# Optimization experiments

Hardware: AMD Instinct MI355X
Metric: run time of the kernel (lower is better)

## Reference

```python
import jax, jax.numpy as jnp
import numpy as np

EMB = 256
HEADS = 8
D_HEAD = EMB // HEADS


def apply_rope(x):
    # x: [B, H, T, D] (interleaved-pair RoPE, matching the torch source)
    T, D = x.shape[-2], x.shape[-1]
    freqs = 10000.0 ** (-jnp.arange(0, D, 2, dtype=jnp.float32) / D)  # [D/2]
    angles = jnp.arange(T, dtype=jnp.float32)[:, None] * freqs[None, :]  # [T, D/2]
    sin = jnp.repeat(jnp.sin(angles), 2, axis=1)  # [T, D]
    cos = jnp.repeat(jnp.cos(angles), 2, axis=1)  # [T, D]
    x1 = x[..., 0::2]
    x2 = x[..., 1::2]
    rotated = jnp.stack((-x2, x1), axis=-1).reshape(x.shape)  # interleave (-x2, x1)
    return x * cos + rotated * sin


def setup_inputs() -> dict:
    key = jax.random.key(0)
    k1, k2, k3, k4, k5 = jax.random.split(key, 5)
    B, T = 8, 2048
    x = jax.random.normal(k1, (B, T, EMB), dtype=jnp.float32)
    s = 1.0 / np.sqrt(EMB)
    # Linear weights stored as [in, out] (torch weight.T), y = x @ W + b
    Wqkv = jax.random.uniform(k2, (EMB, 3 * EMB), minval=-s, maxval=s, dtype=jnp.float32)
    bqkv = jax.random.uniform(k3, (3 * EMB,), minval=-s, maxval=s, dtype=jnp.float32)
    Wout = jax.random.uniform(k4, (EMB, EMB), minval=-s, maxval=s, dtype=jnp.float32)
    bout = jax.random.uniform(k5, (EMB,), minval=-s, maxval=s, dtype=jnp.float32)
    return {"x": x, "Wqkv": Wqkv, "bqkv": bqkv, "Wout": Wout, "bout": bout}


def reference(x, Wqkv, bqkv, Wout, bout):
    B, T, E = x.shape
    H, Dh = HEADS, D_HEAD
    qkv = x @ Wqkv + bqkv  # [B, T, 3E]
    qkv = qkv.reshape(B, T, 3, H, Dh).transpose(2, 0, 3, 1, 4)  # [3, B, H, T, Dh]
    q, k, v = qkv[0], qkv[1], qkv[2]
    q = apply_rope(q)
    k = apply_rope(k)
    scores = jnp.einsum('bhtd,bhsd->bhts', q, k) / np.sqrt(Dh)  # [B, H, T, T]
    causal = jnp.triu(jnp.ones((T, T), dtype=bool), k=1)
    scores = jnp.where(causal, -jnp.inf, scores)
    attn = jax.nn.softmax(scores, axis=-1)
    out = jnp.einsum('bhts,bhsd->bthd', attn, v).reshape(B, T, E)
    return out @ Wout + bout
```

## Files before the change

kernel.cpp:

```cpp
#include <hip/hip_runtime.h>
#include <hip/hip_bf16.h>
#include <math.h>

typedef __hip_bfloat16 bf16;
using s8v = __attribute__((ext_vector_type(8))) short;
using f4v = __attribute__((ext_vector_type(4))) float;
using u32x2 = __attribute__((ext_vector_type(2))) unsigned int;

#if __has_builtin(__builtin_amdgcn_exp2f)
#define EXP2(x) __builtin_amdgcn_exp2f(x)
#else
#define EXP2(x) exp2f(x)
#endif

__device__ __forceinline__ float bfb2f(unsigned short u) {
    return __uint_as_float(((unsigned int)u) << 16);
}
__device__ __forceinline__ unsigned short f2bfb(float f) {
    unsigned int u = __float_as_uint(f);
    unsigned int r = (u + 0x7fffu + ((u >> 16) & 1u)) >> 16;
    return (unsigned short)r;
}
__device__ __forceinline__ unsigned int packbf2_rne(float a, float b) {
    return (unsigned int)f2bfb(a) | ((unsigned int)f2bfb(b) << 16);
}
__device__ __forceinline__ unsigned int packbf2(float a, float b) {
    return __builtin_amdgcn_perm(__float_as_uint(b) + 0x8000u,
                                 __float_as_uint(a) + 0x8000u,
                                 0x07060302u);
}
__device__ __forceinline__ s8v mk8(unsigned int a, unsigned int b,
                                   unsigned int c, unsigned int d) {
    union { unsigned int u[4]; s8v v; } x;
    x.u[0] = a; x.u[1] = b; x.u[2] = c; x.u[3] = d;
    return x.v;
}
__device__ __forceinline__ void plswap(unsigned int& a, unsigned int& b) {
    u32x2 t = __builtin_amdgcn_permlane32_swap(a, b, false, false);
    u32x2 u = __builtin_amdgcn_permlane16_swap(t.x, t.y, false, false);
    a = u.x;
    b = u.y;
}

__device__ __forceinline__ void gload_lds16(const void* g, void* l) {
    __builtin_amdgcn_global_load_lds(
        (const __attribute__((address_space(1))) unsigned int*)g,
        (__attribute__((address_space(3))) unsigned int*)l, 16, 0, 0);
}

__device__ __forceinline__ int sniff_fp32(const void* p, int tid, int* s_flag)
{
    if (tid == 0) *s_flag = 0;
    __syncthreads();
    const uint4* u = (const uint4*)p;
    int local = 0;
    #pragma unroll
    for (int i = 0; i < 4; i++) {
        const uint4 v = u[i * 256 + tid];
        if ((v.x & 0x7F80u) == 0x7F80u) local = 1;
        if ((v.y & 0x7F80u) == 0x7F80u) local = 1;
        if ((v.z & 0x7F80u) == 0x7F80u) local = 1;
        if ((v.w & 0x7F80u) == 0x7F80u) local = 1;
    }
    if (local) atomicOr(s_flag, 1);
    __syncthreads();
    return *s_flag;
}

__global__ __launch_bounds__(256)
void k_prep(const void* __restrict__ x, const void* __restrict__ Wqkv,
            const void* __restrict__ bqkv, const void* __restrict__ Wout,
            const void* __restrict__ bout,
            bf16* __restrict__ wqkvT, bf16* __restrict__ woutT,
            float* __restrict__ bq_f, float* __restrict__ bo_f,
            bf16* __restrict__ xb)
{
    __shared__ int sf;
    const int bid = blockIdx.x;
    const int tid = threadIdx.x;
    if (bid < 768) {
        const int f = sniff_fp32(Wqkv, tid, &sf);
        unsigned short v = f ? f2bfb(((const float*)Wqkv)[(size_t)tid * 768 + bid])
                             : ((const unsigned short*)Wqkv)[(size_t)tid * 768 + bid];
        ((unsigned short*)wqkvT)[(size_t)bid * 256 + tid] = v;
        if (bid < 12) {
            const int i = bid * 256 + tid;
            bq_f[i] = f ? ((const float*)bqkv)[i]
                        : bfb2f(((const unsigned short*)bqkv)[i]);
        }
    } else if (bid < 1024) {
        const int n = bid - 768;
        const int f = sniff_fp32(Wout, tid, &sf);
        unsigned short v = f ? f2bfb(((const float*)Wout)[(size_t)tid * 256 + n])
                             : ((const unsigned short*)Wout)[(size_t)tid * 256 + n];
        ((unsigned short*)woutT)[(size_t)n * 256 + tid] = v;
        if (n == 0)
            bo_f[tid] = f ? ((const float*)bout)[tid]
                          : bfb2f(((const unsigned short*)bout)[tid]);
    } else {
        const int f = sniff_fp32(x, tid, &sf);
        if (f) {
            const size_t cb = (size_t)(bid - 1024) * 4096;
            #pragma unroll
            for (int i = 0; i < 4; i++) {
                const size_t e = cb + (size_t)i * 1024 + tid * 4;
                const float4 v = *(const float4*)((const float*)x + e);
                ushort4 o4;
                o4.x = f2bfb(v.x);
                o4.y = f2bfb(v.y);
                o4.z = f2bfb(v.z);
                o4.w = f2bfb(v.w);
                *(ushort4*)((unsigned short*)xb + e) = o4;
            }
        } else {
            const size_t base = (size_t)(bid - 1024) * 4096 + (size_t)tid * 16;
            const uint4* xu = (const uint4*)((const unsigned short*)x + base);
            uint4* dp = (uint4*)((unsigned short*)xb + base);
            dp[0] = xu[0];
            dp[1] = xu[1];
        }
    }
}

__global__ __launch_bounds__(256)
void k_qkv_rope(const bf16* __restrict__ xb, const bf16* __restrict__ wqkvT,
                const float* __restrict__ bq_f,
                bf16* __restrict__ q_ws, bf16* __restrict__ k_ws,
                bf16* __restrict__ vT_ws)
{
    __shared__ __align__(16) unsigned short Bls[4][8][512];
    __shared__ __align__(16) unsigned short Tls[4][1536];

    const int tid = threadIdx.x;
    const int bx = blockIdx.x;
    const int by = blockIdx.y;
    const int n0 = bx * 64;

    const int w    = tid >> 6;
    const int lane = tid & 63;
    const int col  = lane & 15;
    const int quad = lane >> 4;
    const int which = n0 >> 8;
    const int b     = (by * 128) >> 11;
    unsigned short* Tw = Tls[w];

    #pragma unroll
    for (int kk = 0; kk < 8; kk++)
        gload_lds16((const unsigned short*)wqkvT +
                        (size_t)(n0 + w * 16 + col) * 256 + kk * 32 + quad * 8,
                    &Bls[w][kk][0]);
    __syncthreads();

    const int T0 = by * 128 + w * 32;

    f4v acc[2][4] = {{{0.f,0.f,0.f,0.f}, {0.f,0.f,0.f,0.f},
                      {0.f,0.f,0.f,0.f}, {0.f,0.f,0.f,0.f}},
                     {{0.f,0.f,0.f,0.f}, {0.f,0.f,0.f,0.f},
                      {0.f,0.f,0.f,0.f}, {0.f,0.f,0.f,0.f}}};

    #pragma unroll
    for (int kk = 0; kk < 8; kk++) {
        const s8v av0 = *(const s8v*)((const unsigned short*)xb +
                        (size_t)(T0 + col) * 256 + kk * 32 + quad * 8);
        const s8v av1 = *(const s8v*)((const unsigned short*)xb +
                        (size_t)(T0 + 16 + col) * 256 + kk * 32 + quad * 8);
        #pragma unroll
        for (int c = 0; c < 4; c++) {
            const s8v bv = *(const s8v*)&Bls[c][kk][lane * 8];
            acc[0][c] = __builtin_amdgcn_mfma_f32_16x16x32_bf16(av0, bv, acc[0][c], 0, 0, 0);
            acc[1][c] = __builtin_amdgcn_mfma_f32_16x16x32_bf16(av1, bv, acc[1][c], 0, 0, 0);
        }
    }

    #pragma unroll
    for (int g = 0; g < 2; g++) {
        const int t_base = ((by * 128) & 2047) + w * 32 + g * 16;

        if (which == 2) {
            #pragma unroll
            for (int c = 0; c < 4; c++) {
                const int nl = c * 16 + col;
                const float bias = bq_f[n0 + nl];
                uint2 ww;
                ww.x = packbf2_rne(acc[g][c][0] + bias, acc[g][c][1] + bias);
                ww.y = packbf2_rne(acc[g][c][2] + bias, acc[g][c][3] + bias);
                *(uint2*)(Tw + nl * 24 + quad * 4) = ww;
            }
            const int ng = n0 + lane;
            const int h = (ng & 255) >> 5;
            const int d = ng & 31;
            const s8v t0 = *(const s8v*)&Tw[lane * 24];
            const s8v t1 = *(const s8v*)&Tw[lane * 24 + 8];
            unsigned short* dp = (unsigned short*)vT_ws +
                ((size_t)(b * 8 + h) * 32 + d) * 2048 + t_base;
            *(s8v*)dp = t0;
            *(s8v*)(dp + 8) = t1;
        } else {
            #pragma unroll
            for (int c = 0; c < 4; c++) {
                const int nl = c * 16 + col;
                const int d = (n0 + nl) & 31;
                const float bias = bq_f[n0 + nl];
                const float frev = __expf(-0.28782314f * (float)(d & ~1))
                                 * 0.15915494309189535f;
                #pragma unroll
                for (int r = 0; r < 4; r++) {
                    const float v = acc[g][c][r] + bias;
                    const float vp = __shfl_xor(v, 1);
                    const int t = t_base + quad * 4 + r;
                    float rev = (float)t * frev;
                    rev -= floorf(rev);
                    const float ang = rev * 6.283185307179586f;
                    const float sn = __sinf(ang);
                    const float cs = __cosf(ang);
                    float o = (d & 1) ? (v * cs + vp * sn)
                                      : (v * cs - vp * sn);
                    if (which == 0) o *= 0.25503487021228657f;
                    Tw[(quad * 4 + r) * 80 + nl] = f2bfb(o);
                }
            }
            const int row = lane >> 2;
            const int ch  = lane & 3;
            const int ng  = n0 + ch * 16;
            const int h   = (ng & 255) >> 5;
            const int d   = ng & 31;
            const int t   = t_base + row;
            const s8v t0 = *(const s8v*)&Tw[row * 80 + ch * 16];
            const s8v t1 = *(const s8v*)&Tw[row * 80 + ch * 16 + 8];
            unsigned short* dp = (unsigned short*)(which ? k_ws : q_ws) +
                ((size_t)(b * 8 + h) * 2048 + t) * 32 + d;
            *(s8v*)dp = t0;
            *(s8v*)(dp + 8) = t1;
        }
    }
}

__global__ __launch_bounds__(256, 4)
void k_attn(const bf16* __restrict__ q_ws, const bf16* __restrict__ k_ws,
            const bf16* __restrict__ vT_ws, bf16* __restrict__ ctx)
{
    __shared__ __align__(16) unsigned short KVls[2][8][512];

    const int tid  = threadIdx.x;
    const int w    = tid >> 6;
    const int lane = tid & 63;
    const int col  = lane & 15;
    const int quad = lane >> 4;

    const int idx = blockIdx.x;
    const int bh  = idx & 63;
    const int mb  = 31 - (idx >> 6);
    const int T0  = mb * 64 + w * 16;

    const bf16* qb = q_ws  + (size_t)bh * 65536;
    const bf16* kb = k_ws  + (size_t)bh * 65536;
    const bf16* vb = vT_ws + (size_t)bh * 65536;

    const bf16* kg = kb + (size_t)(w * 16 + col) * 32 + quad * 8;
    const bf16* vg = vb + (size_t)(col + (w & 1) * 16) * 2048
                        + (w >> 1) * 32 + quad * 8;

    const s8v qa = *(const s8v*)(qb + (size_t)(T0 + col) * 32 + quad * 8);

    f4v o0 = {0.f,0.f,0.f,0.f}, o1 = {0.f,0.f,0.f,0.f};
    float lp[4] = {0.f,0.f,0.f,0.f};

    gload_lds16(kg, &KVls[0][w][0]);
    gload_lds16(vg, &KVls[0][4 + w][0]);
    __syncthreads();

    int cur = 0;
    for (int kt = 0; kt <= mb; kt++) {
        const int s0 = kt * 64;

        if (kt < mb) {
            gload_lds16(kg + (size_t)(kt + 1) * 2048, &KVls[cur ^ 1][w][0]);
            gload_lds16(vg + (kt + 1) * 64,           &KVls[cur ^ 1][4 + w][0]);
        }

        const s8v kf0 = *(const s8v*)&KVls[cur][0][lane * 8];
        const s8v kf1 = *(const s8v*)&KVls[cur][1][lane * 8];
        const s8v kf2 = *(const s8v*)&KVls[cur][2][lane * 8];
        const s8v kf3 = *(const s8v*)&KVls[cur][3][lane * 8];
        const s8v v00 = *(const s8v*)&KVls[cur][4][lane * 8];
        const s8v v10 = *(const s8v*)&KVls[cur][5][lane * 8];
        const s8v v01 = *(const s8v*)&KVls[cur][6][lane * 8];
        const s8v v11 = *(const s8v*)&KVls[cur][7][lane * 8];

        const f4v z = {0.f, 0.f, 0.f, 0.f};
        f4v s[4];
        s[0] = __builtin_amdgcn_mfma_f32_16x16x32_bf16(kf0, qa, z, 0, 0, 0);
        s[1] = __builtin_amdgcn_mfma_f32_16x16x32_bf16(kf1, qa, z, 0, 0, 0);
        s[2] = __builtin_amdgcn_mfma_f32_16x16x32_bf16(kf2, qa, z, 0, 0, 0);
        s[3] = __builtin_amdgcn_mfma_f32_16x16x32_bf16(kf3, qa, z, 0, 0, 0);

        if (kt == mb) {
            #pragma unroll
            for (int c = 0; c < 4; c++) {
                const int sbase = s0 + c * 16 + quad * 4;
                #pragma unroll
                for (int r = 0; r < 4; r++)
                    if (sbase + r > T0 + col) s[c][r] = -INFINITY;
            }
        }

        unsigned int pw[8];
        #pragma unroll
        for (int c = 0; c < 4; c++) {
            const float p0 = EXP2(s[c][0]);
            const float p1 = EXP2(s[c][1]);
            const float p2 = EXP2(s[c][2]);
            const float p3 = EXP2(s[c][3]);
            lp[0] += p0; lp[1] += p1; lp[2] += p2; lp[3] += p3;
            pw[c * 2]     = packbf2(p0, p1);
            pw[c * 2 + 1] = packbf2(p2, p3);
        }

        plswap(pw[0], pw[2]);
        plswap(pw[1], pw[3]);
        plswap(pw[4], pw[6]);
        plswap(pw[5], pw[7]);
        const s8v pa0 = mk8(pw[0], pw[1], pw[2], pw[3]);
        const s8v pa1 = mk8(pw[4], pw[5], pw[6], pw[7]);

        o0 = __builtin_amdgcn_mfma_f32_16x16x32_bf16(pa0, v00, o0, 0, 0, 0);
        o1 = __builtin_amdgcn_mfma_f32_16x16x32_bf16(pa0, v10, o1, 0, 0, 0);
        o0 = __builtin_amdgcn_mfma_f32_16x16x32_bf16(pa1, v01, o0, 0, 0, 0);
        o1 = __builtin_amdgcn_mfma_f32_16x16x32_bf16(pa1, v11, o1, 0, 0, 0);

        __syncthreads();
        cur ^= 1;
    }

    float rs = lp[0] + lp[1] + lp[2] + lp[3];
    rs += __shfl_xor(rs, 16);
    rs += __shfl_xor(rs, 32);

    const int b = bh >> 3;
    const int h = bh & 7;
    unsigned short* cp = (unsigned short*)ctx;
    #pragma unroll
    for (int r = 0; r < 4; r++) {
        const float inv = 1.0f / __shfl(rs, quad * 4 + r);
        const float e0 = o0[r] * inv;
        const float e1 = o1[r] * inv;
        const int t = T0 + quad * 4 + r;
        unsigned short* dst = cp + (size_t)(b * 2048 + t) * 256 + h * 32;
        dst[col]      = f2bfb(e0);
        dst[col + 16] = f2bfb(e1);
    }
}

__global__ __launch_bounds__(256)
void k_outproj(const bf16* __restrict__ ctx, const bf16* __restrict__ woutT,
               const float* __restrict__ bo_f, float* __restrict__ out)
{
    __shared__ __align__(16) unsigned short Bls[4][8][512];

    const int tid = threadIdx.x;
    const int bx = blockIdx.x;
    const int by = blockIdx.y;
    const int n0 = bx * 64;

    const int w    = tid >> 6;
    const int lane = tid & 63;
    const int col  = lane & 15;
    const int quad = lane >> 4;

    #pragma unroll
    for (int kk = 0; kk < 8; kk++)
        gload_lds16((const unsigned short*)woutT +
                        (size_t)(n0 + w * 16 + col) * 256 + kk * 32 + quad * 8,
                    &Bls[w][kk][0]);
    __syncthreads();

    const int T0 = by * 128 + w * 32;

    f4v acc[2][4] = {{{0.f,0.f,0.f,0.f}, {0.f,0.f,0.f,0.f},
                      {0.f,0.f,0.f,0.f}, {0.f,0.f,0.f,0.f}},
                     {{0.f,0.f,0.f,0.f}, {0.f,0.f,0.f,0.f},
                      {0.f,0.f,0.f,0.f}, {0.f,0.f,0.f,0.f}}};

    #pragma unroll
    for (int kk = 0; kk < 8; kk++) {
        const s8v av0 = *(const s8v*)((const unsigned short*)ctx +
                        (size_t)(T0 + col) * 256 + kk * 32 + quad * 8);
        const s8v av1 = *(const s8v*)((const unsigned short*)ctx +
                        (size_t)(T0 + 16 + col) * 256 + kk * 32 + quad * 8);
        #pragma unroll
        for (int c = 0; c < 4; c++) {
            const s8v bv = *(const s8v*)&Bls[c][kk][lane * 8];
            acc[0][c] = __builtin_amdgcn_mfma_f32_16x16x32_bf16(av0, bv, acc[0][c], 0, 0, 0);
            acc[1][c] = __builtin_amdgcn_mfma_f32_16x16x32_bf16(av1, bv, acc[1][c], 0, 0, 0);
        }
    }

    #pragma unroll
    for (int g = 0; g < 2; g++) {
        #pragma unroll
        for (int c = 0; c < 4; c++) {
            const int n = n0 + c * 16 + col;
            const float bias = bo_f[n];
            #pragma unroll
            for (int r = 0; r < 4; r++)
                out[(size_t)(T0 + g * 16 + quad * 4 + r) * 256 + n] =
                    acc[g][c][r] + bias;
        }
    }
}

extern "C" void kernel_launch(void* const* d_in, const int* in_sizes, int n_in,
                              void* d_out, int out_size, void* d_ws, size_t ws_size,
                              hipStream_t stream)
{
    const void* x    = d_in[0];
    const void* Wqkv = d_in[1];
    const void* bqkv = d_in[2];
    const void* Wout = d_in[3];
    const void* bout = d_in[4];
    float* out = (float*)d_out;

    const size_t NQ = (size_t)8 * 8 * 2048 * 32;
    bf16* q_ws   = (bf16*)d_ws;
    bf16* k_ws   = q_ws + NQ;
    bf16* vT_ws  = k_ws + NQ;
    bf16* ctx    = vT_ws + NQ;
    bf16* xb     = ctx;
    bf16* wqkvT  = ctx + NQ;
    bf16* woutT  = wqkvT + (size_t)768 * 256;
    float* bq_f  = (float*)(woutT + (size_t)256 * 256);
    float* bo_f  = bq_f + 3072;

    k_prep    <<<2048,          256, 0, stream>>>(x, Wqkv, bqkv, Wout, bout,
                                                  wqkvT, woutT, bq_f, bo_f, xb);
    k_qkv_rope<<<dim3(12, 128), 256, 0, stream>>>(xb, wqkvT, bq_f,
                                                  q_ws, k_ws, vT_ws);
    k_attn    <<<2048,          256, 0, stream>>>(q_ws, k_ws, vT_ws, ctx);
    k_outproj <<<dim3(4, 128),  256, 0, stream>>>(ctx, woutT, bo_f, out);
}
```

Measured before the change: 147.9 us.

## Process 128 query rows per attention block to reuse each K/V tile

New measurement: 149.8 us. Within noise of the previous version (+1.3%).

```diff
diff --git a/kernel.cpp b/kernel.cpp
--- a/kernel.cpp
+++ b/kernel.cpp
@@ -249,8 +249,8 @@
 
     const int idx = blockIdx.x;
     const int bh  = idx & 63;
-    const int mb  = 31 - (idx >> 6);
-    const int T0  = mb * 64 + w * 16;
+    const int mb  = 15 - (idx >> 6);
+    const int T0  = mb * 128 + w * 32;
 
     const bf16* qb = q_ws  + (size_t)bh * 65536;
     const bf16* kb = k_ws  + (size_t)bh * 65536;
@@ -260,94 +260,148 @@
     const bf16* vg = vb + (size_t)(col + (w & 1) * 16) * 2048
                         + (w >> 1) * 32 + quad * 8;
 
-    const s8v qa = *(const s8v*)(qb + (size_t)(T0 + col) * 32 + quad * 8);
-
-    f4v o0 = {0.f,0.f,0.f,0.f}, o1 = {0.f,0.f,0.f,0.f};
-    float lp[4] = {0.f,0.f,0.f,0.f};
+    const s8v qa0 = *(const s8v*)(qb + (size_t)(T0 + col) * 32 + quad * 8);
+    const s8v qa1 = *(const s8v*)(qb + (size_t)(T0 + 16 + col) * 32 + quad * 8);
+
+    f4v o00 = {0.f,0.f,0.f,0.f}, o01 = {0.f,0.f,0.f,0.f};
+    f4v o10 = {0.f,0.f,0.f,0.f}, o11 = {0.f,0.f,0.f,0.f};
+    float lp0[4] = {0.f,0.f,0.f,0.f};
+    float lp1[4] = {0.f,0.f,0.f,0.f};
 
     gload_lds16(kg, &KVls[0][w][0]);
     gload_lds16(vg, &KVls[0][4 + w][0]);
     __syncthreads();
 
+    const int ktmax = 2 * mb + 1;
     int cur = 0;
-    for (int kt = 0; kt <= mb; kt++) {
+    for (int kt = 0; kt <= ktmax; kt++) {
         const int s0 = kt * 64;
 
-        if (kt < mb) {
+        if (kt < ktmax) {
             gload_lds16(kg + (size_t)(kt + 1) * 2048, &KVls[cur ^ 1][w][0]);
             gload_lds16(vg + (kt + 1) * 64,           &KVls[cur ^ 1][4 + w][0]);
         }
 
-        const s8v kf0 = *(const s8v*)&KVls[cur][0][lane * 8];
-        const s8v kf1 = *(const s8v*)&KVls[cur][1][lane * 8];
-        const s8v kf2 = *(const s8v*)&KVls[cur][2][lane * 8];
-        const s8v kf3 = *(const s8v*)&KVls[cur][3][lane * 8];
-        const s8v v00 = *(const s8v*)&KVls[cur][4][lane * 8];
-        const s8v v10 = *(const s8v*)&KVls[cur][5][lane * 8];
-        const s8v v01 = *(const s8v*)&KVls[cur][6][lane * 8];
-        const s8v v11 = *(const s8v*)&KVls[cur][7][lane * 8];
-
-        const f4v z = {0.f, 0.f, 0.f, 0.f};
-        f4v s[4];
-        s[0] = __builtin_amdgcn_mfma_f32_16x16x32_bf16(kf0, qa, z, 0, 0, 0);
-        s[1] = __builtin_amdgcn_mfma_f32_16x16x32_bf16(kf1, qa, z, 0, 0, 0);
-        s[2] = __builtin_amdgcn_mfma_f32_16x16x32_bf16(kf2, qa, z, 0, 0, 0);
-        s[3] = __builtin_amdgcn_mfma_f32_16x16x32_bf16(kf3, qa, z, 0, 0, 0);
-
-        if (kt == mb) {
-            #pragma unroll
-            for (int c = 0; c < 4; c++) {
-                const int sbase = s0 + c * 16 + quad * 4;
+        const bool a0 = (s0 <= T0 + 15);
+        const bool a1 = (s0 <= T0 + 31);
+
+        if (a1) {
+            const s8v kf0 = *(const s8v*)&KVls[cur][0][lane * 8];
+            const s8v kf1 = *(const s8v*)&KVls[cur][1][lane * 8];
+            const s8v kf2 = *(const s8v*)&KVls[cur][2][lane * 8];
+            const s8v kf3 = *(const s8v*)&KVls[cur][3][lane * 8];
+            const s8v v00 = *(const s8v*)&KVls[cur][4][lane * 8];
+            const s8v v10 = *(const s8v*)&KVls[cur][5][lane * 8];
+            const s8v v01 = *(const s8v*)&KVls[cur][6][lane * 8];
+            const s8v v11 = *(const s8v*)&KVls[cur][7][lane * 8];
+
+            const f4v z = {0.f, 0.f, 0.f, 0.f};
+
+            {
+                f4v s[4];
+                s[0] = __builtin_amdgcn_mfma_f32_16x16x32_bf16(kf0, qa1, z, 0, 0, 0);
+                s[1] = __builtin_amdgcn_mfma_f32_16x16x32_bf16(kf1, qa1, z, 0, 0, 0);
+                s[2] = __builtin_amdgcn_mfma_f32_16x16x32_bf16(kf2, qa1, z, 0, 0, 0);
+                s[3] = __builtin_amdgcn_mfma_f32_16x16x32_bf16(kf3, qa1, z, 0, 0, 0);
+                if (s0 + 63 > T0 + 16) {
+                    #pragma unroll
+                    for (int c = 0; c < 4; c++) {
+                        const int sbase = s0 + c * 16 + quad * 4;
+                        #pragma unroll
+                        for (int r = 0; r < 4; r++)
+                            if (sbase + r > T0 + 16 + col) s[c][r] = -INFINITY;
+                    }
+                }
+                unsigned int pw[8];
                 #pragma unroll
-                for (int r = 0; r < 4; r++)
-                    if (sbase + r > T0 + col) s[c][r] = -INFINITY;
+                for (int c = 0; c < 4; c++) {
+                    const float p0 = EXP2(s[c][0]);
+                    const float p1 = EXP2(s[c][1]);
+                    const float p2 = EXP2(s[c][2]);
+                    const float p3 = EXP2(s[c][3]);
+                    lp1[0] += p0; lp1[1] += p1; lp1[2] += p2; lp1[3] += p3;
+                    pw[c * 2]     = packbf2(p0, p1);
+                    pw[c * 2 + 1] = packbf2(p2, p3);
+                }
+                plswap(pw[0], pw[2]);
+                plswap(pw[1], pw[3]);
+                plswap(pw[4], pw[6]);
+                plswap(pw[5], pw[7]);
+                const s8v pa0 = mk8(pw[0], pw[1], pw[2], pw[3]);
+                const s8v pa1 = mk8(pw[4], pw[5], pw[6], pw[7]);
+                o10 = __builtin_amdgcn_mfma_f32_16x16x32_bf16(pa0, v00, o10, 0, 0, 0);
+                o11 = __builtin_amdgcn_mfma_f32_16x16x32_bf16(pa0, v10, o11, 0, 0, 0);
+                o10 = __builtin_amdgcn_mfma_f32_16x16x32_bf16(pa1, v01, o10, 0, 0, 0);
+                o11 = __builtin_amdgcn_mfma_f32_16x16x32_bf16(pa1, v11, o11, 0, 0, 0);
             }
-        }
-
-        unsigned int pw[8];
-        #pragma unroll
-        for (int c = 0; c < 4; c++) {
-            const float p0 = EXP2(s[c][0]);
-            const float p1 = EXP2(s[c][1]);
-            const float p2 = EXP2(s[c][2]);
-            const float p3 = EXP2(s[c][3]);
-            lp[0] += p0; lp[1] += p1; lp[2] += p2; lp[3] += p3;
-            pw[c * 2]     = packbf2(p0, p1);
-            pw[c * 2 + 1] = packbf2(p2, p3);
-        }
-
-        plswap(pw[0], pw[2]);
-        plswap(pw[1], pw[3]);
-        plswap(pw[4], pw[6]);
-        plswap(pw[5], pw[7]);
-        const s8v pa0 = mk8(pw[0], pw[1], pw[2], pw[3]);
-        const s8v pa1 = mk8(pw[4], pw[5], pw[6], pw[7]);
-
-        o0 = __builtin_amdgcn_mfma_f32_16x16x32_bf16(pa0, v00, o0, 0, 0, 0);
-        o1 = __builtin_amdgcn_mfma_f32_16x16x32_bf16(pa0, v10, o1, 0, 0, 0);
-        o0 = __builtin_amdgcn_mfma_f32_16x16x32_bf16(pa1, v01, o0, 0, 0, 0);
-        o1 = __builtin_amdgcn_mfma_f32_16x16x32_bf16(pa1, v11, o1, 0, 0, 0);
+
+            if (a0) {
+                f4v s[4];
+                s[0] = __builtin_amdgcn_mfma_f32_16x16x32_bf16(kf0, qa0, z, 0, 0, 0);
+                s[1] = __builtin_amdgcn_mfma_f32_16x16x32_bf16(kf1, qa0, z, 0, 0, 0);
+                s[2] = __builtin_amdgcn_mfma_f32_16x16x32_bf16(kf2, qa0, z, 0, 0, 0);
+                s[3] = __builtin_amdgcn_mfma_f32_16x16x32_bf16(kf3, qa0, z, 0, 0, 0);
+                if (s0 + 63 > T0) {
+                    #pragma unroll
+                    for (int c = 0; c < 4; c++) {
+                        const int sbase = s0 + c * 16 + quad * 4;
+                        #pragma unroll
+                        for (int r = 0; r < 4; r++)
+                            if (sbase + r > T0 + col) s[c][r] = -INFINITY;
+                    }
+                }
+                unsigned int pw[8];
+                #pragma unroll
+                for (int c = 0; c < 4; c++) {
+                    const float p0 = EXP2(s[c][0]);
+                    const float p1 = EXP2(s[c][1]);
+                    const float p2 = EXP2(s[c][2]);
+                    const float p3 = EXP2(s[c][3]);
+                    lp0[0] += p0; lp0[1] += p1; lp0[2] += p2; lp0[3] += p3;
+                    pw[c * 2]     = packbf2(p0, p1);
+                    pw[c * 2 + 1] = packbf2(p2, p3);
+                }
+                plswap(pw[0], pw[2]);
+                plswap(pw[1], pw[3]);
+                plswap(pw[4], pw[6]);
+                plswap(pw[5], pw[7]);
+                const s8v pa0 = mk8(pw[0], pw[1], pw[2], pw[3]);
+                const s8v pa1 = mk8(pw[4], pw[5], pw[6], pw[7]);
+                o00 = __builtin_amdgcn_mfma_f32_16x16x32_bf16(pa0, v00, o00, 0, 0, 0);
+                o01 = __builtin_amdgcn_mfma_f32_16x16x32_bf16(pa0, v10, o01, 0, 0, 0);
+                o00 = __builtin_amdgcn_mfma_f32_16x16x32_bf16(pa1, v01, o00, 0, 0, 0);
+                o01 = __builtin_amdgcn_mfma_f32_16x16x32_bf16(pa1, v11, o01, 0, 0, 0);
+            }
+        }
 
         __syncthreads();
         cur ^= 1;
     }
 
-    float rs = lp[0] + lp[1] + lp[2] + lp[3];
-    rs += __shfl_xor(rs, 16);
-    rs += __shfl_xor(rs, 32);
+    float rs0 = lp0[0] + lp0[1] + lp0[2] + lp0[3];
+    rs0 += __shfl_xor(rs0, 16);
+    rs0 += __shfl_xor(rs0, 32);
+    float rs1 = lp1[0] + lp1[1] + lp1[2] + lp1[3];
+    rs1 += __shfl_xor(rs1, 16);
+    rs1 += __shfl_xor(rs1, 32);
 
     const int b = bh >> 3;
     const int h = bh & 7;
     unsigned short* cp = (unsigned short*)ctx;
     #pragma unroll
-    for (int r = 0; r < 4; r++) {
-        const float inv = 1.0f / __shfl(rs, quad * 4 + r);
-        const float e0 = o0[r] * inv;
-        const float e1 = o1[r] * inv;
-        const int t = T0 + quad * 4 + r;
-        unsigned short* dst = cp + (size_t)(b * 2048 + t) * 256 + h * 32;
-        dst[col]      = f2bfb(e0);
-        dst[col + 16] = f2bfb(e1);
+    for (int g = 0; g < 2; g++) {
+        const float rs = g ? rs1 : rs0;
+        const int T0g = T0 + g * 16;
+        #pragma unroll
+        for (int r = 0; r < 4; r++) {
+            const float inv = 1.0f / __shfl(rs, quad * 4 + r);
+            const float e0 = (g ? o10[r] : o00[r]) * inv;
+            const float e1 = (g ? o11[r] : o01[r]) * inv;
+            const int t = T0g + quad * 4 + r;
+            unsigned short* dst = cp + (size_t)(b * 2048 + t) * 256 + h * 32;
+            dst[col]      = f2bfb(e0);
+            dst[col + 16] = f2bfb(e1);
+        }
     }
 }
 
@@ -435,6 +489,6 @@
                                                   wqkvT, woutT, bq_f, bo_f, xb);
     k_qkv_rope<<<dim3(12, 128), 256, 0, stream>>>(xb, wqkvT, bq_f,
                                                   q_ws, k_ws, vT_ws);
-    k_attn    <<<2048,          256, 0, stream>>>(q_ws, k_ws, vT_ws, ctx);
+    k_attn    <<<1024,          256, 0, stream>>>(q_ws, k_ws, vT_ws, ctx);
     k_outproj <<<dim3(4, 128),  256, 0, stream>>>(ctx, woutT, bo_f, out);
 }
```
